# Kernel tuning notes

Measured on AMD Instinct MI355X. Metric: run time of the kernel, lower is better.

Reference implementation:

```python
import jax, jax.numpy as jnp
import numpy as np

TOP_K = 2
NUM_EXPERTS = 64


def setup_inputs() -> dict:
    key = jax.random.key(0)
    k1, k2 = jax.random.split(key)
    bs, sq, h = 4, 4096, 4096
    x = jax.random.normal(k1, (bs, sq, h), dtype=jnp.float32)
    expert_mask = jnp.ones((bs, NUM_EXPERTS), dtype=jnp.float32)
    # router weight: torch.nn.Linear(hidden, num_experts, bias=False) -> [E, H]
    W = jax.random.normal(k2, (NUM_EXPERTS, h), dtype=jnp.float32) * 0.02
    return {"x": x, "expert_mask": expert_mask, "W": W}


def reference(x, expert_mask, W):
    bs, sq, h = x.shape
    # logits = Linear(x.view(-1, h)) : [bs*sq, E]
    logits = jnp.einsum("bsh,eh->bse", x, W).reshape(bs * sq, NUM_EXPERTS)
    scores = jax.nn.softmax(logits, axis=-1)
    # expert_mask [bs, E] broadcast over seq
    scores = (expert_mask[:, None, :] * scores.reshape(bs, sq, NUM_EXPERTS)).reshape(
        bs * sq, NUM_EXPERTS
    )
    expert_weights, expert_indices = jax.lax.top_k(scores, TOP_K)  # [bs*sq, k]
    expert_weights = jax.nn.softmax(expert_weights, axis=-1)
    # moe_normalize_expert_weights = 1 -> L1 norm renormalization
    expert_weights = expert_weights / jnp.sum(
        jnp.abs(expert_weights), axis=-1, keepdims=True
    )
    return scores, logits, expert_weights, expert_indices
```

## Files before the change

### kernel.cpp

```cpp
#include <hip/hip_runtime.h>
#include <hip/hip_bf16.h>

#define NE     64
#define HDIM   4096
#define NTOK   16384
#define KSPLIT 8
#define KPER   (HDIM / KSPLIT)
#define KC     32
#define NT     (KPER / KC)
#define NCHUNK (HDIM / 32)
#define TOKB   128
#define PT     130

typedef __attribute__((ext_vector_type(8))) short bf16x8;
typedef __attribute__((ext_vector_type(4))) float f32x4;

union FragU { uint4 u; bf16x8 v; };

__device__ __forceinline__ unsigned rne_bf16(float f) {
    unsigned v = __float_as_uint(f);
    return (v + 0x7FFFu + ((v >> 16) & 1u)) >> 16;
}

__device__ __forceinline__ void split8f(const float* s, FragU& hi, FragU& lo) {
#pragma unroll
    for (int w = 0; w < 4; ++w) {
        const unsigned u0 = __float_as_uint(s[2 * w]);
        const unsigned u1 = __float_as_uint(s[2 * w + 1]);
        const unsigned h0 = u0 & 0xFFFF0000u, h1 = u1 & 0xFFFF0000u;
        ((unsigned*)&hi.u)[w] = (h0 >> 16) | h1;
        const float l0 = __uint_as_float(u0) - __uint_as_float(h0);
        const float l1 = __uint_as_float(u1) - __uint_as_float(h1);
        ((unsigned*)&lo.u)[w] = rne_bf16(l0) | (rne_bf16(l1) << 16);
    }
}

__global__ __launch_bounds__(256) void prep_w(
    const float* __restrict__ W, uint4* __restrict__ wfh, uint4* __restrict__ wfl) {
    const int idx = blockIdx.x * 256 + threadIdx.x;
    const int l  = idx & 63;
    const int ce = idx >> 6;
    const int e  = ce & 3;
    const int c  = ce >> 2;
    const float* src = W + (size_t)(e * 16 + (l & 15)) * HDIM + c * 32 + (l >> 4) * 8;

    unsigned hw[4], lw[4];
#pragma unroll
    for (int w = 0; w < 4; ++w) {
        const float x0 = src[2 * w], x1 = src[2 * w + 1];
        const unsigned u0 = __float_as_uint(x0), u1 = __float_as_uint(x1);
        const unsigned h0 = u0 & 0xFFFF0000u, h1 = u1 & 0xFFFF0000u;
        hw[w] = (h0 >> 16) | h1;
        const float l0 = x0 - __uint_as_float(h0);
        const float l1 = x1 - __uint_as_float(h1);
        lw[w] = rne_bf16(l0) | (rne_bf16(l1) << 16);
    }
    wfh[idx] = make_uint4(hw[0], hw[1], hw[2], hw[3]);
    wfl[idx] = make_uint4(lw[0], lw[1], lw[2], lw[3]);
}

#define MFMA_STEP(AH0, AL0, AH1, AL1, WH, WL)                                          \
    _Pragma("unroll")                                                                   \
    for (int e = 0; e < 4; ++e) {                                                       \
        acc[0][e] = __builtin_amdgcn_mfma_f32_16x16x32_bf16(AH0.v, WH[e].v, acc[0][e], 0, 0, 0); \
        acc[0][e] = __builtin_amdgcn_mfma_f32_16x16x32_bf16(AL0.v, WH[e].v, acc[0][e], 0, 0, 0); \
        acc[0][e] = __builtin_amdgcn_mfma_f32_16x16x32_bf16(AH0.v, WL[e].v, acc[0][e], 0, 0, 0); \
        acc[1][e] = __builtin_amdgcn_mfma_f32_16x16x32_bf16(AH1.v, WH[e].v, acc[1][e], 0, 0, 0); \
        acc[1][e] = __builtin_amdgcn_mfma_f32_16x16x32_bf16(AL1.v, WH[e].v, acc[1][e], 0, 0, 0); \
        acc[1][e] = __builtin_amdgcn_mfma_f32_16x16x32_bf16(AH1.v, WL[e].v, acc[1][e], 0, 0, 0); \
    }

__global__ __launch_bounds__(256) void gemm_logits_mfma(
    const float* __restrict__ x, const uint4* __restrict__ wfh,
    const uint4* __restrict__ wfl, float* __restrict__ part0,
    float* __restrict__ wspart) {
    __shared__ float xs[2][KC][PT];

    const int tid  = threadIdx.x;
    const int lane = tid & 63;
    const int wv   = tid >> 6;
    const int t0   = blockIdx.x * TOKB;
    const int bk   = blockIdx.y;
    const int r    = lane & 15;
    const int u    = lane >> 4;

    f32x4 acc[2][4];
#pragma unroll
    for (int f = 0; f < 2; ++f)
#pragma unroll
        for (int e = 0; e < 4; ++e) acc[f][e] = (f32x4){0.f, 0.f, 0.f, 0.f};

    const int srow = tid >> 3;
    const int skq  = tid & 7;
    const float* gsrc = x + (size_t)(t0 + srow) * HDIM + bk * KPER + skq * 4;

    const uint4* whb = wfh + (size_t)(bk * NT) * 256 + lane;
    const uint4* wlb = wfl + (size_t)(bk * NT) * 256 + lane;

    float4 ldE[4], ldO[4];
    FragU WhA[4], WlA[4], WhB[4], WlB[4];

#define LOADT(LD, T)                                                              \
    _Pragma("unroll")                                                             \
    for (int p = 0; p < 4; ++p)                                                   \
        LD[p] = *reinterpret_cast<const float4*>(gsrc + (size_t)(32 * p) * HDIM + (T) * KC);

#define WRITET(B, LD)                                                             \
    _Pragma("unroll")                                                             \
    for (int p = 0; p < 4; ++p) {                                                 \
        const int rr = srow + 32 * p;                                             \
        xs[B][skq * 4 + 0][rr] = LD[p].x;                                         \
        xs[B][skq * 4 + 1][rr] = LD[p].y;                                         \
        xs[B][skq * 4 + 2][rr] = LD[p].z;                                         \
        xs[B][skq * 4 + 3][rr] = LD[p].w;                                         \
    }

#define COMPUTE(B, WH, WL_)                                                       \
    {                                                                             \
        float a0[8], a1[8];                                                       \
        const float* xb = &xs[B][0][0] + (u * 8) * PT + crow;                     \
        _Pragma("unroll")                                                         \
        for (int j = 0; j < 8; ++j) { a0[j] = xb[j * PT]; a1[j] = xb[j * PT + 16]; } \
        FragU ah0, al0, ah1, al1;                                                 \
        split8f(a0, ah0, al0);                                                    \
        split8f(a1, ah1, al1);                                                    \
        MFMA_STEP(ah0, al0, ah1, al1, WH, WL_)                                    \
    }

    const int crow = wv * 32 + r;

#pragma unroll
    for (int e = 0; e < 4; ++e) { WhA[e].u = whb[e * 64]; WlA[e].u = wlb[e * 64]; }
    LOADT(ldE, 0)
    LOADT(ldO, 1)
    WRITET(0, ldE)
    LOADT(ldE, 2)
    __syncthreads();

    for (int t2 = 0; t2 < NT; t2 += 2) {
        {
            const size_t c = (size_t)(t2 + 1) * 256;
#pragma unroll
            for (int e = 0; e < 4; ++e) { WhB[e].u = whb[c + e * 64]; WlB[e].u = wlb[c + e * 64]; }
            WRITET(1, ldO)
            if (t2 + 3 < NT) { LOADT(ldO, t2 + 3) }
            COMPUTE(0, WhA, WlA)
            __syncthreads();
        }
        {
            const int tn = t2 + 2;
            if (tn < NT) {
                const size_t c = (size_t)tn * 256;
#pragma unroll
                for (int e = 0; e < 4; ++e) { WhA[e].u = whb[c + e * 64]; WlA[e].u = wlb[c + e * 64]; }
                WRITET(0, ldE)
                if (t2 + 4 < NT) { LOADT(ldE, t2 + 4) }
            }
            COMPUTE(1, WhB, WlB)
            if (tn < NT) { __syncthreads(); }
        }
    }

    float* dst = (bk == 0 ? part0 : wspart + (size_t)(bk - 1) * NTOK * NE);
#pragma unroll
    for (int f = 0; f < 2; ++f)
#pragma unroll
        for (int e = 0; e < 4; ++e)
#pragma unroll
            for (int rr = 0; rr < 4; ++rr)
                dst[(size_t)(t0 + wv * 32 + f * 16 + u * 4 + rr) * NE + e * 16 + r] = acc[f][e][rr];
#undef LOADT
#undef WRITET
#undef COMPUTE
}

__global__ __launch_bounds__(256) void router_kernel(
    const float* __restrict__ wspart, const float* __restrict__ mask,
    float* __restrict__ out, int ksplit) {
    const int lane = threadIdx.x & 63;
    const int wv   = threadIdx.x >> 6;
    const int t    = blockIdx.x * 4 + wv;

    float* lo = out + (size_t)NTOK * NE + (size_t)t * NE;
    float l = lo[lane];
    for (int c = 1; c < ksplit; ++c)
        l += wspart[((size_t)(c - 1) * NTOK + t) * NE + lane];
    lo[lane] = l;

    float mx = l;
#pragma unroll
    for (int m = 32; m; m >>= 1) mx = fmaxf(mx, __shfl_xor(mx, m, 64));
    const float ev = __expf(l - mx);
    float s = ev;
#pragma unroll
    for (int m = 32; m; m >>= 1) s += __shfl_xor(s, m, 64);
    const float sc = mask[(size_t)(t >> 12) * NE + lane] * (ev / s);
    out[(size_t)t * NE + lane] = sc;

    const unsigned long long key =
        ((unsigned long long)__float_as_uint(sc) << 6) | (unsigned long long)(63 - lane);
    unsigned long long k1 = key;
#pragma unroll
    for (int m = 32; m; m >>= 1) {
        const unsigned long long o = __shfl_xor(k1, m, 64);
        if (o > k1) k1 = o;
    }
    const int   i1 = 63 - (int)(k1 & 63ull);
    const float v1 = __uint_as_float((unsigned)(k1 >> 6));

    unsigned long long k2 = (lane == i1) ? 0ull : key;
#pragma unroll
    for (int m = 32; m; m >>= 1) {
        const unsigned long long o = __shfl_xor(k2, m, 64);
        if (o > k2) k2 = o;
    }
    const int   i2 = 63 - (int)(k2 & 63ull);
    const float v2 = __uint_as_float((unsigned)(k2 >> 6));

    if (lane == 0) {
        const float e2v = __expf(v2 - v1);
        float w1 = 1.f / (1.f + e2v);
        float w2 = e2v / (1.f + e2v);
        const float sw = w1 + w2;
        w1 /= sw; w2 /= sw;
        const size_t wo = (size_t)2 * NTOK * NE;
        out[wo + (size_t)t * 2 + 0] = w1;
        out[wo + (size_t)t * 2 + 1] = w2;
        const size_t io = wo + (size_t)NTOK * 2;
        out[io + (size_t)t * 2 + 0] = (float)i1;
        out[io + (size_t)t * 2 + 1] = (float)i2;
    }
}

extern "C" void kernel_launch(void* const* d_in, const int* in_sizes, int n_in,
                              void* d_out, int out_size, void* d_ws, size_t ws_size,
                              hipStream_t stream) {
    const float* x    = (const float*)d_in[0];
    const float* mask = (const float*)d_in[1];
    const float* W    = (const float*)d_in[2];
    float* out = (float*)d_out;
    float* ws  = (float*)d_ws;

    float* wspart = ws;
    uint4* wfh = (uint4*)(ws + (size_t)(KSPLIT - 1) * NTOK * NE);
    uint4* wfl = wfh + (size_t)NCHUNK * 4 * 64;
    float* part0 = out + (size_t)NTOK * NE;

    prep_w<<<dim3(NCHUNK * 4 * 64 / 256), dim3(256), 0, stream>>>(W, wfh, wfl);
    gemm_logits_mfma<<<dim3(NTOK / TOKB, KSPLIT), dim3(256), 0, stream>>>(
        x, wfh, wfl, part0, wspart);
    router_kernel<<<dim3(NTOK / 4), dim3(256), 0, stream>>>(wspart, mask, out, KSPLIT);
}
```

Measured before the change: 83.80 us.

## Shrink token tile to 64 and use row-major LDS layout with K chunk 64

Halves the tokens per block (128 to 64) and doubles the K step per stage (32 to 64). The LDS tile for x becomes row-major with padding 67, and each wave now handles 16 tokens instead of 32. Weight fragments are loaded inside the compute step instead of being double-buffered in registers. The aim is more blocks and better occupancy with fewer registers per thread. In exchange, each weight fragment is reused across half as many tokens, so weight traffic per token rises, and the stride-67 LDS reads may cause bank conflicts.

```diff
diff --git a/kernel.cpp b/kernel.cpp
--- a/kernel.cpp
+++ b/kernel.cpp
@@ -6,11 +6,11 @@
 #define NTOK   16384
 #define KSPLIT 8
 #define KPER   (HDIM / KSPLIT)
-#define KC     32
+#define KC     64
 #define NT     (KPER / KC)
 #define NCHUNK (HDIM / 32)
-#define TOKB   128
-#define PT     130
+#define TOKB   64
+#define PK     67
 
 typedef __attribute__((ext_vector_type(8))) short bf16x8;
 typedef __attribute__((ext_vector_type(4))) float f32x4;
@@ -59,22 +59,11 @@
     wfl[idx] = make_uint4(lw[0], lw[1], lw[2], lw[3]);
 }
 
-#define MFMA_STEP(AH0, AL0, AH1, AL1, WH, WL)                                          \
-    _Pragma("unroll")                                                                   \
-    for (int e = 0; e < 4; ++e) {                                                       \
-        acc[0][e] = __builtin_amdgcn_mfma_f32_16x16x32_bf16(AH0.v, WH[e].v, acc[0][e], 0, 0, 0); \
-        acc[0][e] = __builtin_amdgcn_mfma_f32_16x16x32_bf16(AL0.v, WH[e].v, acc[0][e], 0, 0, 0); \
-        acc[0][e] = __builtin_amdgcn_mfma_f32_16x16x32_bf16(AH0.v, WL[e].v, acc[0][e], 0, 0, 0); \
-        acc[1][e] = __builtin_amdgcn_mfma_f32_16x16x32_bf16(AH1.v, WH[e].v, acc[1][e], 0, 0, 0); \
-        acc[1][e] = __builtin_amdgcn_mfma_f32_16x16x32_bf16(AL1.v, WH[e].v, acc[1][e], 0, 0, 0); \
-        acc[1][e] = __builtin_amdgcn_mfma_f32_16x16x32_bf16(AH1.v, WL[e].v, acc[1][e], 0, 0, 0); \
-    }
-
 __global__ __launch_bounds__(256) void gemm_logits_mfma(
     const float* __restrict__ x, const uint4* __restrict__ wfh,
     const uint4* __restrict__ wfl, float* __restrict__ part0,
     float* __restrict__ wspart) {
-    __shared__ float xs[2][KC][PT];
+    __shared__ float xs[2][TOKB][PK];
 
     const int tid  = threadIdx.x;
     const int lane = tid & 63;
@@ -83,54 +72,59 @@
     const int bk   = blockIdx.y;
     const int r    = lane & 15;
     const int u    = lane >> 4;
-
-    f32x4 acc[2][4];
-#pragma unroll
-    for (int f = 0; f < 2; ++f)
-#pragma unroll
-        for (int e = 0; e < 4; ++e) acc[f][e] = (f32x4){0.f, 0.f, 0.f, 0.f};
-
-    const int srow = tid >> 3;
-    const int skq  = tid & 7;
-    const float* gsrc = x + (size_t)(t0 + srow) * HDIM + bk * KPER + skq * 4;
-
-    const uint4* whb = wfh + (size_t)(bk * NT) * 256 + lane;
-    const uint4* wlb = wfl + (size_t)(bk * NT) * 256 + lane;
+    const int crow = wv * 16 + r;
+
+    f32x4 acc[4];
+#pragma unroll
+    for (int e = 0; e < 4; ++e) acc[e] = (f32x4){0.f, 0.f, 0.f, 0.f};
+
+    const int srow = tid >> 4;
+    const int scol = tid & 15;
+    const float* gsrc = x + (size_t)(t0 + srow) * HDIM + bk * KPER + scol * 4;
+
+    const uint4* whb = wfh + (size_t)(bk * (KPER / 32)) * 256 + lane;
+    const uint4* wlb = wfl + (size_t)(bk * (KPER / 32)) * 256 + lane;
 
     float4 ldE[4], ldO[4];
-    FragU WhA[4], WlA[4], WhB[4], WlB[4];
 
 #define LOADT(LD, T)                                                              \
     _Pragma("unroll")                                                             \
     for (int p = 0; p < 4; ++p)                                                   \
-        LD[p] = *reinterpret_cast<const float4*>(gsrc + (size_t)(32 * p) * HDIM + (T) * KC);
+        LD[p] = *reinterpret_cast<const float4*>(gsrc + (size_t)(16 * p) * HDIM + (T) * KC);
 
 #define WRITET(B, LD)                                                             \
     _Pragma("unroll")                                                             \
     for (int p = 0; p < 4; ++p) {                                                 \
-        const int rr = srow + 32 * p;                                             \
-        xs[B][skq * 4 + 0][rr] = LD[p].x;                                         \
-        xs[B][skq * 4 + 1][rr] = LD[p].y;                                         \
-        xs[B][skq * 4 + 2][rr] = LD[p].z;                                         \
-        xs[B][skq * 4 + 3][rr] = LD[p].w;                                         \
-    }
-
-#define COMPUTE(B, WH, WL_)                                                       \
-    {                                                                             \
-        float a0[8], a1[8];                                                       \
-        const float* xb = &xs[B][0][0] + (u * 8) * PT + crow;                     \
+        const int rr = srow + 16 * p;                                             \
+        xs[B][rr][scol * 4 + 0] = LD[p].x;                                        \
+        xs[B][rr][scol * 4 + 1] = LD[p].y;                                        \
+        xs[B][rr][scol * 4 + 2] = LD[p].z;                                        \
+        xs[B][rr][scol * 4 + 3] = LD[p].w;                                        \
+    }
+
+#define COMPUTE(B, T)                                                             \
+    _Pragma("unroll")                                                             \
+    for (int kc = 0; kc < 2; ++kc) {                                              \
+        FragU Wh[4], Wl[4];                                                       \
+        const size_t cb = (size_t)(2 * (T) + kc) * 256;                           \
         _Pragma("unroll")                                                         \
-        for (int j = 0; j < 8; ++j) { a0[j] = xb[j * PT]; a1[j] = xb[j * PT + 16]; } \
-        FragU ah0, al0, ah1, al1;                                                 \
-        split8f(a0, ah0, al0);                                                    \
-        split8f(a1, ah1, al1);                                                    \
-        MFMA_STEP(ah0, al0, ah1, al1, WH, WL_)                                    \
-    }
-
-    const int crow = wv * 32 + r;
-
-#pragma unroll
-    for (int e = 0; e < 4; ++e) { WhA[e].u = whb[e * 64]; WlA[e].u = wlb[e * 64]; }
+        for (int e = 0; e < 4; ++e) {                                             \
+            Wh[e].u = whb[cb + e * 64];                                           \
+            Wl[e].u = wlb[cb + e * 64];                                           \
+        }                                                                         \
+        float a[8];                                                               \
+        _Pragma("unroll")                                                         \
+        for (int j = 0; j < 8; ++j) a[j] = xs[B][crow][kc * 32 + u * 8 + j];      \
+        FragU ah, al;                                                             \
+        split8f(a, ah, al);                                                       \
+        _Pragma("unroll")                                                         \
+        for (int e = 0; e < 4; ++e) {                                             \
+            acc[e] = __builtin_amdgcn_mfma_f32_16x16x32_bf16(ah.v, Wh[e].v, acc[e], 0, 0, 0); \
+            acc[e] = __builtin_amdgcn_mfma_f32_16x16x32_bf16(al.v, Wh[e].v, acc[e], 0, 0, 0); \
+            acc[e] = __builtin_amdgcn_mfma_f32_16x16x32_bf16(ah.v, Wl[e].v, acc[e], 0, 0, 0); \
+        }                                                                         \
+    }
+
     LOADT(ldE, 0)
     LOADT(ldO, 1)
     WRITET(0, ldE)
@@ -139,36 +133,28 @@
 
     for (int t2 = 0; t2 < NT; t2 += 2) {
         {
-            const size_t c = (size_t)(t2 + 1) * 256;
-#pragma unroll
-            for (int e = 0; e < 4; ++e) { WhB[e].u = whb[c + e * 64]; WlB[e].u = wlb[c + e * 64]; }
             WRITET(1, ldO)
             if (t2 + 3 < NT) { LOADT(ldO, t2 + 3) }
-            COMPUTE(0, WhA, WlA)
+            COMPUTE(0, t2)
             __syncthreads();
         }
         {
             const int tn = t2 + 2;
             if (tn < NT) {
-                const size_t c = (size_t)tn * 256;
-#pragma unroll
-                for (int e = 0; e < 4; ++e) { WhA[e].u = whb[c + e * 64]; WlA[e].u = wlb[c + e * 64]; }
                 WRITET(0, ldE)
                 if (t2 + 4 < NT) { LOADT(ldE, t2 + 4) }
             }
-            COMPUTE(1, WhB, WlB)
+            COMPUTE(1, t2 + 1)
             if (tn < NT) { __syncthreads(); }
         }
     }
 
     float* dst = (bk == 0 ? part0 : wspart + (size_t)(bk - 1) * NTOK * NE);
 #pragma unroll
-    for (int f = 0; f < 2; ++f)
-#pragma unroll
-        for (int e = 0; e < 4; ++e)
-#pragma unroll
-            for (int rr = 0; rr < 4; ++rr)
-                dst[(size_t)(t0 + wv * 32 + f * 16 + u * 4 + rr) * NE + e * 16 + r] = acc[f][e][rr];
+    for (int e = 0; e < 4; ++e)
+#pragma unroll
+        for (int rr = 0; rr < 4; ++rr)
+            dst[(size_t)(t0 + wv * 16 + u * 4 + rr) * NE + e * 16 + r] = acc[e][rr];
 #undef LOADT
 #undef WRITET
 #undef COMPUTE
```

Result: slower. 93.24 us (+11.3%).

## Store x tile token-major in LDS with float4 reads/writes and reorder compute

Applied to the files above, without the earlier changes.

The shared-memory x tile changes from a transposed [k][token] layout (scalar stores and strided scalar loads) to a token-major [token][k] layout padded to 36, so each thread writes float4s and reads each fragment as two float4 loads. The split-to-bf16 helper now takes float4 inputs. The loop body also moves the MFMA compute ahead of the LDS write and the next global load, so the matrix work issues before the memory operations. The aim is fewer LDS instructions and fewer bank conflicts, at the cost of some possible conflicts on the 128-bit accesses and longer register lifetimes for the prefetched data.

```diff
diff --git a/kernel.cpp b/kernel.cpp
--- a/kernel.cpp
+++ b/kernel.cpp
@@ -10,7 +10,7 @@
 #define NT     (KPER / KC)
 #define NCHUNK (HDIM / 32)
 #define TOKB   128
-#define PT     130
+#define PK     36
 
 typedef __attribute__((ext_vector_type(8))) short bf16x8;
 typedef __attribute__((ext_vector_type(4))) float f32x4;
@@ -22,11 +22,16 @@
     return (v + 0x7FFFu + ((v >> 16) & 1u)) >> 16;
 }
 
-__device__ __forceinline__ void split8f(const float* s, FragU& hi, FragU& lo) {
+__device__ __forceinline__ void split8(const float4 a, const float4 b,
+                                       FragU& hi, FragU& lo) {
+    const unsigned ue[8] = {
+        __float_as_uint(a.x), __float_as_uint(a.y),
+        __float_as_uint(a.z), __float_as_uint(a.w),
+        __float_as_uint(b.x), __float_as_uint(b.y),
+        __float_as_uint(b.z), __float_as_uint(b.w)};
 #pragma unroll
     for (int w = 0; w < 4; ++w) {
-        const unsigned u0 = __float_as_uint(s[2 * w]);
-        const unsigned u1 = __float_as_uint(s[2 * w + 1]);
+        const unsigned u0 = ue[2 * w], u1 = ue[2 * w + 1];
         const unsigned h0 = u0 & 0xFFFF0000u, h1 = u1 & 0xFFFF0000u;
         ((unsigned*)&hi.u)[w] = (h0 >> 16) | h1;
         const float l0 = __uint_as_float(u0) - __uint_as_float(h0);
@@ -74,7 +79,7 @@
     const float* __restrict__ x, const uint4* __restrict__ wfh,
     const uint4* __restrict__ wfl, float* __restrict__ part0,
     float* __restrict__ wspart) {
-    __shared__ float xs[2][KC][PT];
+    __shared__ float xs[2][TOKB][PK];
 
     const int tid  = threadIdx.x;
     const int lane = tid & 63;
@@ -83,6 +88,7 @@
     const int bk   = blockIdx.y;
     const int r    = lane & 15;
     const int u    = lane >> 4;
+    const int crow = wv * 32 + r;
 
     f32x4 acc[2][4];
 #pragma unroll
@@ -107,27 +113,20 @@
 
 #define WRITET(B, LD)                                                             \
     _Pragma("unroll")                                                             \
-    for (int p = 0; p < 4; ++p) {                                                 \
-        const int rr = srow + 32 * p;                                             \
-        xs[B][skq * 4 + 0][rr] = LD[p].x;                                         \
-        xs[B][skq * 4 + 1][rr] = LD[p].y;                                         \
-        xs[B][skq * 4 + 2][rr] = LD[p].z;                                         \
-        xs[B][skq * 4 + 3][rr] = LD[p].w;                                         \
-    }
+    for (int p = 0; p < 4; ++p)                                                   \
+        *reinterpret_cast<float4*>(&xs[B][srow + 32 * p][skq * 4]) = LD[p];
 
 #define COMPUTE(B, WH, WL_)                                                       \
     {                                                                             \
-        float a0[8], a1[8];                                                       \
-        const float* xb = &xs[B][0][0] + (u * 8) * PT + crow;                     \
-        _Pragma("unroll")                                                         \
-        for (int j = 0; j < 8; ++j) { a0[j] = xb[j * PT]; a1[j] = xb[j * PT + 16]; } \
+        const float4 q0 = *reinterpret_cast<const float4*>(&xs[B][crow][u * 8]);          \
+        const float4 q1 = *reinterpret_cast<const float4*>(&xs[B][crow][u * 8 + 4]);      \
+        const float4 q2 = *reinterpret_cast<const float4*>(&xs[B][crow + 16][u * 8]);     \
+        const float4 q3 = *reinterpret_cast<const float4*>(&xs[B][crow + 16][u * 8 + 4]); \
         FragU ah0, al0, ah1, al1;                                                 \
-        split8f(a0, ah0, al0);                                                    \
-        split8f(a1, ah1, al1);                                                    \
+        split8(q0, q1, ah0, al0);                                                 \
+        split8(q2, q3, ah1, al1);                                                 \
         MFMA_STEP(ah0, al0, ah1, al1, WH, WL_)                                    \
     }
-
-    const int crow = wv * 32 + r;
 
 #pragma unroll
     for (int e = 0; e < 4; ++e) { WhA[e].u = whb[e * 64]; WlA[e].u = wlb[e * 64]; }
@@ -142,9 +141,9 @@
             const size_t c = (size_t)(t2 + 1) * 256;
 #pragma unroll
             for (int e = 0; e < 4; ++e) { WhB[e].u = whb[c + e * 64]; WlB[e].u = wlb[c + e * 64]; }
+            COMPUTE(0, WhA, WlA)
             WRITET(1, ldO)
             if (t2 + 3 < NT) { LOADT(ldO, t2 + 3) }
-            COMPUTE(0, WhA, WlA)
             __syncthreads();
         }
         {
@@ -153,11 +152,13 @@
                 const size_t c = (size_t)tn * 256;
 #pragma unroll
                 for (int e = 0; e < 4; ++e) { WhA[e].u = whb[c + e * 64]; WlA[e].u = wlb[c + e * 64]; }
+            }
+            COMPUTE(1, WhB, WlB)
+            if (tn < NT) {
                 WRITET(0, ldE)
                 if (t2 + 4 < NT) { LOADT(ldE, t2 + 4) }
+                __syncthreads();
             }
-            COMPUTE(1, WhB, WlB)
-            if (tn < NT) { __syncthreads(); }
         }
     }
 
```

Result: slower. 156.4 us (+86.6%).

## Use single 64-wide LDS stage with register prefetch instead of double buffering

Applied to the files above, without the earlier changes.

Doubles the K chunk per LDS phase to 64 and replaces the two-buffer LDS ping-pong with a single buffer. The next chunk is prefetched into registers while the current one is computed. This halves the number of phases but adds a second barrier per phase, so LDS writes no longer overlap compute. It also raises register pressure from the 8 float4 prefetch registers.

```diff
diff --git a/kernel.cpp b/kernel.cpp
--- a/kernel.cpp
+++ b/kernel.cpp
@@ -6,8 +6,8 @@
 #define NTOK   16384
 #define KSPLIT 8
 #define KPER   (HDIM / KSPLIT)
-#define KC     32
-#define NT     (KPER / KC)
+#define KC     64
+#define NPH    (KPER / KC)
 #define NCHUNK (HDIM / 32)
 #define TOKB   128
 #define PT     130
@@ -74,7 +74,7 @@
     const float* __restrict__ x, const uint4* __restrict__ wfh,
     const uint4* __restrict__ wfl, float* __restrict__ part0,
     float* __restrict__ wspart) {
-    __shared__ float xs[2][KC][PT];
+    __shared__ float xs[KC][PT];
 
     const int tid  = threadIdx.x;
     const int lane = tid & 63;
@@ -83,6 +83,7 @@
     const int bk   = blockIdx.y;
     const int r    = lane & 15;
     const int u    = lane >> 4;
+    const int crow = wv * 32 + r;
 
     f32x4 acc[2][4];
 #pragma unroll
@@ -94,31 +95,47 @@
     const int skq  = tid & 7;
     const float* gsrc = x + (size_t)(t0 + srow) * HDIM + bk * KPER + skq * 4;
 
-    const uint4* whb = wfh + (size_t)(bk * NT) * 256 + lane;
-    const uint4* wlb = wfl + (size_t)(bk * NT) * 256 + lane;
-
-    float4 ldE[4], ldO[4];
+    const uint4* whb = wfh + (size_t)(bk * (KPER / 32)) * 256 + lane;
+    const uint4* wlb = wfl + (size_t)(bk * (KPER / 32)) * 256 + lane;
+
+    float4 ld[8];
     FragU WhA[4], WlA[4], WhB[4], WlB[4];
 
-#define LOADT(LD, T)                                                              \
+#define LOADT(T)                                                                  \
     _Pragma("unroll")                                                             \
-    for (int p = 0; p < 4; ++p)                                                   \
-        LD[p] = *reinterpret_cast<const float4*>(gsrc + (size_t)(32 * p) * HDIM + (T) * KC);
-
-#define WRITET(B, LD)                                                             \
+    for (int p = 0; p < 4; ++p) {                                                 \
+        ld[2 * p]     = *reinterpret_cast<const float4*>(gsrc + (size_t)(32 * p) * HDIM + (T) * KC);      \
+        ld[2 * p + 1] = *reinterpret_cast<const float4*>(gsrc + (size_t)(32 * p) * HDIM + (T) * KC + 32); \
+    }
+
+#define WRITET()                                                                  \
     _Pragma("unroll")                                                             \
     for (int p = 0; p < 4; ++p) {                                                 \
         const int rr = srow + 32 * p;                                             \
-        xs[B][skq * 4 + 0][rr] = LD[p].x;                                         \
-        xs[B][skq * 4 + 1][rr] = LD[p].y;                                         \
-        xs[B][skq * 4 + 2][rr] = LD[p].z;                                         \
-        xs[B][skq * 4 + 3][rr] = LD[p].w;                                         \
-    }
-
-#define COMPUTE(B, WH, WL_)                                                       \
+        xs[skq * 4 + 0][rr] = ld[2 * p].x;                                        \
+        xs[skq * 4 + 1][rr] = ld[2 * p].y;                                        \
+        xs[skq * 4 + 2][rr] = ld[2 * p].z;                                        \
+        xs[skq * 4 + 3][rr] = ld[2 * p].w;                                        \
+        xs[32 + skq * 4 + 0][rr] = ld[2 * p + 1].x;                               \
+        xs[32 + skq * 4 + 1][rr] = ld[2 * p + 1].y;                               \
+        xs[32 + skq * 4 + 2][rr] = ld[2 * p + 1].z;                               \
+        xs[32 + skq * 4 + 3][rr] = ld[2 * p + 1].w;                               \
+    }
+
+#define LOADW(WH, WL_, CC)                                                        \
+    {                                                                             \
+        const size_t c_ = (size_t)(CC) * 256;                                     \
+        _Pragma("unroll")                                                         \
+        for (int e = 0; e < 4; ++e) {                                             \
+            WH[e].u = whb[c_ + e * 64];                                           \
+            WL_[e].u = wlb[c_ + e * 64];                                          \
+        }                                                                         \
+    }
+
+#define COMPUTE(KCC, WH, WL_)                                                     \
     {                                                                             \
         float a0[8], a1[8];                                                       \
-        const float* xb = &xs[B][0][0] + (u * 8) * PT + crow;                     \
+        const float* xb = &xs[(KCC) * 32][0] + (u * 8) * PT + crow;               \
         _Pragma("unroll")                                                         \
         for (int j = 0; j < 8; ++j) { a0[j] = xb[j * PT]; a1[j] = xb[j * PT + 16]; } \
         FragU ah0, al0, ah1, al1;                                                 \
@@ -127,37 +144,21 @@
         MFMA_STEP(ah0, al0, ah1, al1, WH, WL_)                                    \
     }
 
-    const int crow = wv * 32 + r;
-
-#pragma unroll
-    for (int e = 0; e < 4; ++e) { WhA[e].u = whb[e * 64]; WlA[e].u = wlb[e * 64]; }
-    LOADT(ldE, 0)
-    LOADT(ldO, 1)
-    WRITET(0, ldE)
-    LOADT(ldE, 2)
+    LOADT(0)
+    WRITET()
+    LOADW(WhA, WlA, 0)
     __syncthreads();
 
-    for (int t2 = 0; t2 < NT; t2 += 2) {
-        {
-            const size_t c = (size_t)(t2 + 1) * 256;
-#pragma unroll
-            for (int e = 0; e < 4; ++e) { WhB[e].u = whb[c + e * 64]; WlB[e].u = wlb[c + e * 64]; }
-            WRITET(1, ldO)
-            if (t2 + 3 < NT) { LOADT(ldO, t2 + 3) }
-            COMPUTE(0, WhA, WlA)
+    for (int T = 0; T < NPH; ++T) {
+        if (T + 1 < NPH) { LOADT(T + 1) }
+        LOADW(WhB, WlB, 2 * T + 1)
+        COMPUTE(0, WhA, WlA)
+        if (2 * T + 2 < KPER / 32) { LOADW(WhA, WlA, 2 * T + 2) }
+        COMPUTE(1, WhB, WlB)
+        if (T + 1 < NPH) {
             __syncthreads();
-        }
-        {
-            const int tn = t2 + 2;
-            if (tn < NT) {
-                const size_t c = (size_t)tn * 256;
-#pragma unroll
-                for (int e = 0; e < 4; ++e) { WhA[e].u = whb[c + e * 64]; WlA[e].u = wlb[c + e * 64]; }
-                WRITET(0, ldE)
-                if (t2 + 4 < NT) { LOADT(ldE, t2 + 4) }
-            }
-            COMPUTE(1, WhB, WlB)
-            if (tn < NT) { __syncthreads(); }
+            WRITET()
+            __syncthreads();
         }
     }
 
@@ -171,6 +172,7 @@
                 dst[(size_t)(t0 + wv * 32 + f * 16 + u * 4 + rr) * NE + e * 16 + r] = acc[f][e][rr];
 #undef LOADT
 #undef WRITET
+#undef LOADW
 #undef COMPUTE
 }
 
```

Result: no change. 84.87 us (+1.3%).
